# Performance work log

Hardware: AMD Instinct MI355X
Metric: run time of the kernel (lower is better)

The kernel has to match this reference:

```python
import jax, jax.numpy as jnp
import numpy as np

GROUPS = 32
EPS = 1e-5
NUM_HEADS = 8

def group_norm(x, scale, bias):
    # x: [N, C, T], GroupNorm(32) as in diffusion normalization()
    N, C, T = x.shape
    xg = x.reshape(N, GROUPS, -1)
    mean = xg.mean(-1, keepdims=True)
    var = xg.var(-1, keepdims=True)
    xg = (xg - mean) * jax.lax.rsqrt(var + EPS)
    return xg.reshape(N, C, T) * scale[None, :, None] + bias[None, :, None]


def setup_inputs() -> dict:
    key = jax.random.key(0)
    ks = jax.random.split(key, 10)
    B, D, C, T, TE = 2, 32, 256, 64, 1024
    s = 0.02
    inp = {}
    inp["x"] = jax.random.normal(ks[0], (B, D, C, T), jnp.float32)
    inp["temb"] = jax.random.normal(ks[1], (B, TE, T), jnp.float32)
    inp["frame_indices"] = jnp.sort(jax.random.randint(ks[2], (B, T), 0, 1000), axis=-1)
    inp["attn_mask"] = jnp.ones((B, T), jnp.float32)
    inp["norm_scale"] = jnp.ones((C,), jnp.float32)
    inp["norm_bias"] = jnp.zeros((C,), jnp.float32)
    inp["w_qkv"] = jax.random.normal(ks[3], (3 * C, C), jnp.float32) * s
    inp["b_qkv"] = jnp.zeros((3 * C,), jnp.float32)
    inp["w_aug1"] = jax.random.normal(ks[4], (C, 3), jnp.float32) * s
    inp["b_aug1"] = jnp.zeros((C,), jnp.float32)
    inp["w_aug2"] = jax.random.normal(ks[5], (C, TE), jnp.float32) * s
    inp["b_aug2"] = jnp.zeros((C,), jnp.float32)
    inp["w_aug3"] = jax.random.normal(ks[6], (C, C), jnp.float32) * s
    inp["b_aug3"] = jnp.zeros((C,), jnp.float32)
    inp["w_proj"] = jax.random.normal(ks[7], (C, C), jnp.float32) * s
    inp["b_proj"] = jnp.zeros((C,), jnp.float32)
    return inp


def reference(x, temb, frame_indices, attn_mask, norm_scale, norm_bias,
              w_qkv, b_qkv, w_aug1, b_aug1, w_aug2, b_aug2, w_aug3, b_aug3,
              w_proj, b_proj):
    B, D, C, T = x.shape
    H = NUM_HEADS
    cph = C // H  # channels per head
    # norm + 1x1 qkv conv over channels
    h = group_norm(x.reshape(B * D, C, T), norm_scale, norm_bias)
    qkv = jnp.einsum('nct,oc->not', h, w_qkv) + b_qkv[None, :, None]
    qkv = qkv.reshape(B, D, 3, cph, H, T)
    q, k, v = qkv[:, :, 0], qkv[:, :, 1], qkv[:, :, 2]
    scale = 1.0 / np.sqrt(np.sqrt(cph))
    w = jnp.einsum('bdcht,bdchs->bdhts', q * scale, k * scale)  # [B,D,H,T,T]
    # relative-position features: [B,3,T,T]
    rel = frame_indices[:, None, None, :] - frame_indices[:, None, :, None]
    rel3 = jnp.concatenate([
        jnp.clip(rel, 0, None).astype(jnp.float32),
        jnp.clip(-rel, 0, None).astype(jnp.float32),
        (rel == 0).astype(jnp.float32)], axis=1)
    rel3 = jnp.log1p(rel3)
    emb = jnp.einsum('bits,oi->bots', rel3, w_aug1) + b_aug1[None, :, None, None]  # [B,C,T,T]
    emb = emb + (jnp.einsum('bet,oe->bot', temb, w_aug2) + b_aug2[None, :, None])[:, :, :, None]
    wa = jnp.einsum('bits,oi->bots', jax.nn.relu(emb), w_aug3) + b_aug3[None, :, None, None]
    # tile heads into full channel dim (matches torch .repeat ordering) and add bias pre-softmax
    w = jnp.tile(w, (1, 1, cph, 1, 1)) + wa[:, None]  # [B,D,C,T,T]
    w = jnp.where(attn_mask[:, None, None, None, :] > 0, w, -jnp.inf)
    w = jax.nn.softmax(w.astype(jnp.float32), axis=-1).astype(x.dtype)
    hv = jnp.einsum('bdcts,bdcs->bdct', w, v.reshape(B, D, C, T))
    out = x + jnp.einsum('bdct,oc->bdot', hv, w_proj) + b_proj[None, None, :, None]
    return out
```

## Files before the change

### kernel.cpp

```cpp
#include <hip/hip_runtime.h>

#define B_ 2
#define D_ 32
#define C_ 256
#define T_ 64
#define TE_ 1024
#define H_ 8
#define N_ 64

typedef __attribute__((ext_vector_type(8))) short bf16x8;
typedef __attribute__((ext_vector_type(8))) unsigned short u16x8;
typedef __attribute__((ext_vector_type(4))) float f32x4;

__device__ inline ushort f2bf(float x){
  unsigned u = __float_as_uint(x);
  unsigned r = u + 0x7FFFu + ((u>>16)&1u);
  return (ushort)(r>>16);
}
__device__ inline float bf2f(ushort u){
  return __uint_as_float(((unsigned)u)<<16);
}

__global__ __launch_bounds__(256) void k_prep(
    const float* __restrict__ w_qkv, const float* __restrict__ wp,
    const float* __restrict__ w3,
    ushort* __restrict__ wqb, ushort* __restrict__ wpr, ushort* __restrict__ w3b,
    const float* __restrict__ x, const float* __restrict__ nsc,
    const float* __restrict__ nbi, ushort* __restrict__ ht,
    const float* __restrict__ temb, const float* __restrict__ w2,
    const float* __restrict__ b2, float* __restrict__ tp)
{
  __shared__ float smem[5120];
  int blk = blockIdx.x;
  int tid = threadIdx.x;
  if (blk < 320) {
    if (blk < 192) {
      int i = blk*256 + tid;
      float4 v = ((const float4*)w_qkv)[i];
      ushort4 o; o.x=f2bf(v.x); o.y=f2bf(v.y); o.z=f2bf(v.z); o.w=f2bf(v.w);
      ((ushort4*)wqb)[i] = o;
    } else if (blk < 256) {
      int i = (blk-192)*256 + tid;
      float4 v = ((const float4*)wp)[i];
      int o = i >> 6, c0 = (i & 63)*4;
      #pragma unroll
      for (int e=0;e<4;e++){
        int c = c0+e;
        float vv = (e==0)?v.x:(e==1)?v.y:(e==2)?v.z:v.w;
        wpr[o*256 + (c&7)*32 + (c>>3)] = f2bf(vv);
      }
    } else {
      int i = (blk-256)*256 + tid;
      float4 v = ((const float4*)w3)[i];
      ushort4 o; o.x=f2bf(v.x); o.y=f2bf(v.y); o.z=f2bf(v.z); o.w=f2bf(v.w);
      ((ushort4*)w3b)[i] = o;
    }
    return;
  }
  if (blk < 2368) {
    int b2k = blk - 320;
    int n = b2k >> 5, g = b2k & 31;
    const float* xp = x + ((size_t)n*C_ + g*8) * T_;
    float v0 = xp[tid], v1 = xp[tid+256];
    float s = v0+v1, ss = v0*v0 + v1*v1;
    #pragma unroll
    for (int off=32; off; off>>=1) { s += __shfl_down(s,off); ss += __shfl_down(ss,off); }
    float* red = smem;
    ushort* gbuf = (ushort*)(smem + 16);
    int wid = tid>>6, lane = tid&63;
    if (lane==0){ red[wid]=s; red[4+wid]=ss; }
    __syncthreads();
    if (tid==0){
      float a  = red[0]+red[1]+red[2]+red[3];
      float bb = red[4]+red[5]+red[6]+red[7];
      float mean = a*(1.f/512.f);
      float var  = bb*(1.f/512.f) - mean*mean;
      red[8]=mean; red[9]=rsqrtf(var + 1e-5f);
    }
    __syncthreads();
    float mean = red[8], inv = red[9];
    int t = tid & 63, w = tid >> 6;
    int c0 = g*8 + w, c1 = c0 + 4;
    gbuf[w*64 + t]     = f2bf((v0-mean)*inv*nsc[c0] + nbi[c0]);
    gbuf[(w+4)*64 + t] = f2bf((v1-mean)*inv*nsc[c1] + nbi[c1]);
    __syncthreads();
    if (tid < 64){
      u16x8 pk;
      #pragma unroll
      for (int i=0;i<8;i++) pk[i] = gbuf[i*64 + tid];
      *(u16x8*)&ht[((size_t)n*T_ + tid)*C_ + g*8] = pk;
    }
    return;
  }
  {
    int b3k = blk - 2368;
    int b = b3k >> 6, ob = b3k & 63;
    float* w2s = smem;
    float* red = smem + 4096;
    const float* w2p = w2 + (size_t)ob*4*1024;
    #pragma unroll
    for (int r = 0; r < 16; r++) w2s[r*256 + tid] = w2p[r*256 + tid];
    __syncthreads();
    int t = tid & 63, eq = tid >> 6;
    const float* tep = temb + ((size_t)b*1024 + eq*256)*64 + t;
    const float* wq  = w2s + eq*256;
    float acc[4] = {0.f,0.f,0.f,0.f};
    #pragma unroll 4
    for (int i = 0; i < 256; i += 4) {
      float tv0 = tep[(i+0)*64];
      float tv1 = tep[(i+1)*64];
      float tv2 = tep[(i+2)*64];
      float tv3 = tep[(i+3)*64];
      #pragma unroll
      for (int j = 0; j < 4; j++) {
        float4 w4 = *(const float4*)&wq[j*1024 + i];
        acc[j] = fmaf(w4.x, tv0, acc[j]);
        acc[j] = fmaf(w4.y, tv1, acc[j]);
        acc[j] = fmaf(w4.z, tv2, acc[j]);
        acc[j] = fmaf(w4.w, tv3, acc[j]);
      }
    }
    #pragma unroll
    for (int j=0;j<4;j++) red[(eq*4+j)*64 + t] = acc[j];
    __syncthreads();
    if (tid < 64) {
      #pragma unroll
      for (int j=0;j<4;j++){
        int o = ob*4 + j;
        float v = red[j*64+tid]+red[(4+j)*64+tid]+red[(8+j)*64+tid]+red[(12+j)*64+tid];
        tp[((size_t)b*256+o)*64 + tid] = v + b2[o];
      }
    }
  }
}

__global__ __launch_bounds__(256) void k_mm(
    const ushort* __restrict__ Wb, const ushort* __restrict__ Inb,
    const float* __restrict__ bias, ushort* __restrict__ Out)
{
  int blk = blockIdx.x;
  int n = blk / 12, ob = blk - n*12;
  int tid = threadIdx.x;
  int lane = tid & 63, w = tid >> 6;
  int o0 = ob*64 + w*16;
  int r = lane & 15, kg = lane >> 4;
  const ushort* wp = Wb + (size_t)(o0 + r)*256 + kg*8;
  const ushort* ip = Inb + ((size_t)n*64 + r)*256 + kg*8;
  f32x4 acc[4];
  #pragma unroll
  for (int j=0;j<4;j++) acc[j] = (f32x4){0.f,0.f,0.f,0.f};
  #pragma unroll
  for (int ks = 0; ks < 8; ks++) {
    bf16x8 a = *(const bf16x8*)(wp + ks*32);
    #pragma unroll
    for (int j = 0; j < 4; j++) {
      bf16x8 b = *(const bf16x8*)(ip + (size_t)j*16*256 + ks*32);
      acc[j] = __builtin_amdgcn_mfma_f32_16x16x32_bf16(a, b, acc[j], 0, 0, 0);
    }
  }
  #pragma unroll
  for (int j = 0; j < 4; j++) {
    #pragma unroll
    for (int rr = 0; rr < 4; rr++) {
      int o = o0 + kg*4 + rr;
      size_t idx = ((size_t)n*768 + o)*64 + j*16 + r;
      float v = acc[j][rr] + bias[o];
      if (o < 512) v *= 0.42044820762685725f;
      Out[idx] = f2bf(v);
    }
  }
}

__global__ __launch_bounds__(256) void k_sw(
    const ushort* __restrict__ qkv, ushort* __restrict__ es,
    const float* __restrict__ amask,
    const int* __restrict__ fi, const float* __restrict__ w1,
    const float* __restrict__ b1, const float* __restrict__ tp,
    const ushort* __restrict__ w3b, const float* __restrict__ b3,
    ushort* __restrict__ ew)
{
  __shared__ char smem[33536];
  int blk = blockIdx.x;
  int tid = threadIdx.x;
  if (blk < 512) {
    int n = blk >> 3, hh = blk & 7;
    float* qs = (float*)smem;
    float* ks = qs + 2048;
    const ushort* base = qkv + (size_t)n*(768*64);
    for (int i=tid; i<2048; i+=256){
      int cq = i>>6, tt = i&63;
      qs[i] = bf2f(base[(cq*8+hh)*64 + tt]);
      ks[i] = bf2f(base[(256 + cq*8+hh)*64 + tt]);
    }
    __syncthreads();
    int s  = tid & 63;
    int t4 = __builtin_amdgcn_readfirstlane(tid>>6);
    float msk = amask[(n >> 5)*64 + s];
    float acc[16];
    #pragma unroll
    for (int j=0;j<16;j++) acc[j]=0.f;
    for (int cq=0;cq<32;cq++){
      float kv = ks[cq*64+s];
      #pragma unroll
      for (int j=0;j<16;j++) acc[j] = fmaf(qs[cq*64 + t4*16 + j], kv, acc[j]);
    }
    ushort* op = es + (size_t)blk*4096;
    #pragma unroll
    for (int j=0;j<16;j++)
      op[(t4*16+j)*64 + s] = f2bf(msk > 0.f ? __expf(acc[j]) : 0.f);
    return;
  }
  {
    int blk2 = blk - 512;
    int oh = blk2 & 1; int bt = blk2 >> 1;
    int b = bt >> 6, t = bt & 63;
    float* l0 = (float*)smem;
    float* l1 = l0 + 64;
    float* l2 = l1 + 64;
    ushort* Ebuf = (ushort*)(smem + 768);
    if (tid < 64){
      int rel = fi[b*64+tid] - fi[b*64+t];
      float r0 = rel>0 ? (float)rel   : 0.f;
      float r1 = rel<0 ? (float)(-rel): 0.f;
      l0[tid] = log1pf(r0);
      l1[tid] = log1pf(r1);
      l2[tid] = (rel==0) ? 0.6931471805599453f : 0.f;
    }
    __syncthreads();
    int s = tid & 63;
    int iq = __builtin_amdgcn_readfirstlane(tid >> 6);
    float L0 = l0[s], L1 = l1[s], L2 = l2[s];
    #pragma unroll
    for (int c8 = 0; c8 < 8; c8++){
      int chunk = iq*8 + c8;
      int ibase = chunk*8;
      u16x8 pack;
      #pragma unroll
      for (int e = 0; e < 8; e++){
        int i = ibase + e;
        float bb = b1[i] + tp[((size_t)b*256 + i)*64 + t];
        float evv = fmaf(w1[i*3], L0, fmaf(w1[i*3+1], L1, fmaf(w1[i*3+2], L2, bb)));
        pack[e] = f2bf(fmaxf(evv, 0.f));
      }
      int csw = chunk ^ (s & 31);
      *(u16x8*)&Ebuf[s*256 + csw*8] = pack;
    }
    __syncthreads();
    int lane = tid & 63, w = tid >> 6;
    int r = lane & 15, kg = lane >> 4;
    int o0 = oh*128 + w*32;
    f32x4 acc[2][4];
    #pragma unroll
    for (int m=0;m<2;m++)
      #pragma unroll
      for (int j=0;j<4;j++) acc[m][j] = (f32x4){0.f,0.f,0.f,0.f};
    #pragma unroll
    for (int ks8 = 0; ks8 < 8; ks8++){
      bf16x8 a0 = *(const bf16x8*)(w3b + (size_t)(o0 +      r)*256 + kg*8 + ks8*32);
      bf16x8 a1 = *(const bf16x8*)(w3b + (size_t)(o0 + 16 + r)*256 + kg*8 + ks8*32);
      #pragma unroll
      for (int j=0;j<4;j++){
        int srow = j*16 + r;
        int chunk = (kg + ks8*4) ^ (srow & 31);
        bf16x8 bfr = *(const bf16x8*)&Ebuf[srow*256 + chunk*8];
        acc[0][j] = __builtin_amdgcn_mfma_f32_16x16x32_bf16(a0, bfr, acc[0][j], 0, 0, 0);
        acc[1][j] = __builtin_amdgcn_mfma_f32_16x16x32_bf16(a1, bfr, acc[1][j], 0, 0, 0);
      }
    }
    #pragma unroll
    for (int m=0;m<2;m++){
      #pragma unroll
      for (int j=0;j<4;j++){
        #pragma unroll
        for (int rr=0;rr<4;rr++){
          int o = o0 + m*16 + kg*4 + rr;
          int scol = j*16 + r;
          ew[((size_t)(b*256+o))*4096 + t*64 + scol] = f2bf(__expf(acc[m][j][rr] + b3[o]));
        }
      }
    }
  }
}

__global__ __launch_bounds__(256) void k_attn(
    const ushort* __restrict__ es, const ushort* __restrict__ ew,
    const ushort* __restrict__ qkv, ushort* __restrict__ hv1)
{
  int i = blockIdx.x;
  int xcd = i & 7, j0 = i >> 3;
  int g = xcd + ((j0 >> 6) << 3);
  int w64 = j0 & 63;
  int b = g >> 3, hh = g & 7;
  int dq = w64 >> 3, cs = w64 & 7;
  int tid = threadIdx.x;
  int t  = tid & 63;
  int dj = __builtin_amdgcn_readfirstlane(tid >> 6);
  int n  = b*D_ + dq*4 + dj;
  __shared__ float4 ewl[64][16];
  __shared__ float4 vl4[4][16];
  float4 esr[16];
  {
    const u16x8* sp = (const u16x8*)(es + ((size_t)(n*8 + hh))*4096 + (size_t)t*64);
    #pragma unroll
    for (int k8=0;k8<8;k8++){
      u16x8 e8 = sp[k8];
      float4 lo, hi;
      lo.x=bf2f(e8[0]); lo.y=bf2f(e8[1]); lo.z=bf2f(e8[2]); lo.w=bf2f(e8[3]);
      hi.x=bf2f(e8[4]); hi.y=bf2f(e8[5]); hi.z=bf2f(e8[6]); hi.w=bf2f(e8[7]);
      esr[2*k8] = lo; esr[2*k8+1] = hi;
    }
  }
  int vd = tid >> 4, vk = tid & 15;
  u16x8 rew[2]; ushort4 rv;
  {
    int c = cs*32 + hh;
    const u16x8* wap = (const u16x8*)(ew + ((size_t)(b*256 + c))*4096);
    rew[0] = wap[tid]; rew[1] = wap[tid+256];
    if (tid < 64)
      rv = *(const ushort4*)(qkv + ((size_t)(b*D_ + dq*4 + vd)*768 + 512 + c)*64 + 4*vk);
  }
  for (int ci=0; ci<4; ci++){
    __syncthreads();
    #pragma unroll
    for (int i2=0;i2<2;i2++){
      int ch = tid + 256*i2;
      int tr = ch >> 3, k8 = ch & 7;
      u16x8 e8 = rew[i2];
      float4 lo, hi;
      lo.x=bf2f(e8[0]); lo.y=bf2f(e8[1]); lo.z=bf2f(e8[2]); lo.w=bf2f(e8[3]);
      hi.x=bf2f(e8[4]); hi.y=bf2f(e8[5]); hi.z=bf2f(e8[6]); hi.w=bf2f(e8[7]);
      ewl[tr][(k8*2)   ^ (tr & 15)] = lo;
      ewl[tr][(k8*2+1) ^ (tr & 15)] = hi;
    }
    if (tid < 64){
      float4 vv; vv.x=bf2f(rv.x); vv.y=bf2f(rv.y); vv.z=bf2f(rv.z); vv.w=bf2f(rv.w);
      vl4[vd][vk] = vv;
    }
    __syncthreads();
    if (ci < 3){
      int c = (cs*4 + ci + 1)*8 + hh;
      const u16x8* wap = (const u16x8*)(ew + ((size_t)(b*256 + c))*4096);
      rew[0] = wap[tid]; rew[1] = wap[tid+256];
      if (tid < 64)
        rv = *(const ushort4*)(qkv + ((size_t)(b*D_ + dq*4 + vd)*768 + 512 + c)*64 + 4*vk);
    }
    float sum = 0.f;
    float ax=0.f, ay=0.f, az=0.f, aw=0.f;
    #pragma unroll
    for (int k=0;k<16;k++){
      float4 e4 = esr[k];
      float4 w4 = ewl[t][k ^ (t & 15)];
      float4 v4 = vl4[dj][k];
      float px = e4.x*w4.x, py = e4.y*w4.y, pz = e4.z*w4.z, pw = e4.w*w4.w;
      sum += px+py+pz+pw;
      ax = fmaf(px, v4.x, ax);
      ay = fmaf(py, v4.y, ay);
      az = fmaf(pz, v4.z, az);
      aw = fmaf(pw, v4.w, aw);
    }
    float acc = (ax+ay)+(az+aw);
    int cq = cs*4 + ci;
    hv1[(((size_t)n*8 + hh)*32 + cq)*64 + t] = f2bf(acc / sum);
  }
}

__global__ __launch_bounds__(256) void k_proj(
    const ushort* __restrict__ Wr, const ushort* __restrict__ hv1,
    const float* __restrict__ bias, const float* __restrict__ resid,
    float* __restrict__ Out)
{
  int blk = blockIdx.x;
  int n = blk >> 2, ob = blk & 3;
  int tid = threadIdx.x;
  int lane = tid & 63, w = tid >> 6;
  int o0 = ob*64 + w*16;
  int r = lane & 15, kg = lane >> 4;
  const ushort* wp = Wr + (size_t)(o0 + r)*256 + kg*8;
  f32x4 acc[4];
  #pragma unroll
  for (int j=0;j<4;j++) acc[j] = (f32x4){0.f,0.f,0.f,0.f};
  #pragma unroll
  for (int ks = 0; ks < 8; ks++) {
    bf16x8 a = *(const bf16x8*)(wp + ks*32);
    #pragma unroll
    for (int j = 0; j < 4; j++) {
      const ushort* bp = hv1 + (((size_t)n*8 + ks)*32 + kg*8)*64 + (j*16 + r);
      bf16x8 bfr;
      #pragma unroll
      for (int e=0;e<8;e++) bfr[e] = (short)bp[(size_t)e*64];
      acc[j] = __builtin_amdgcn_mfma_f32_16x16x32_bf16(a, bfr, acc[j], 0, 0, 0);
    }
  }
  #pragma unroll
  for (int j = 0; j < 4; j++) {
    #pragma unroll
    for (int rr = 0; rr < 4; rr++) {
      int o = o0 + kg*4 + rr;
      size_t idx = ((size_t)n*256 + o)*64 + j*16 + r;
      Out[idx] = acc[j][rr] + bias[o] + resid[idx];
    }
  }
}

extern "C" void kernel_launch(void* const* d_in, const int* in_sizes, int n_in,
                              void* d_out, int out_size, void* d_ws, size_t ws_size,
                              hipStream_t stream) {
  const float* x     = (const float*)d_in[0];
  const float* temb  = (const float*)d_in[1];
  const int*   fi    = (const int*)  d_in[2];
  const float* amask = (const float*)d_in[3];
  const float* nsc   = (const float*)d_in[4];
  const float* nbi   = (const float*)d_in[5];
  const float* w_qkv = (const float*)d_in[6];
  const float* b_qkv = (const float*)d_in[7];
  const float* w1    = (const float*)d_in[8];
  const float* b1    = (const float*)d_in[9];
  const float* w2    = (const float*)d_in[10];
  const float* b2    = (const float*)d_in[11];
  const float* w3    = (const float*)d_in[12];
  const float* b3    = (const float*)d_in[13];
  const float* wp    = (const float*)d_in[14];
  const float* bp    = (const float*)d_in[15];
  float* out = (float*)d_out;

  ushort* qkvb = (ushort*)d_ws;
  float*  tpb  = (float*)(qkvb + 3145728);
  ushort* esb  = (ushort*)(tpb + 32768);
  ushort* ewb  = esb + 2097152;
  ushort* htb  = ewb + 2097152;
  ushort* hvb  = htb + 1048576;
  ushort* wqb  = hvb + 1048576;
  ushort* wprb = wqb + 196608;
  ushort* w3b  = wprb + 65536;

  k_prep <<<2496, 256, 0, stream>>>(w_qkv, wp, w3, wqb, wprb, w3b,
                                    x, nsc, nbi, htb, temb, w2, b2, tpb);
  k_mm   <<<N_*12, 256, 0, stream>>>(wqb, htb, b_qkv, qkvb);
  k_sw   <<<768, 256, 0, stream>>>(qkvb, esb, amask, fi, w1, b1, tpb, w3b, b3, ewb);
  k_attn <<<B_*H_*8*8, 256, 0, stream>>>(esb, ewb, qkvb, hvb);
  k_proj <<<N_*4, 256, 0, stream>>>(wprb, hvb, bp, x, out);
}
```

Before: 64.49 us.

## Fuse QK score computation into attention kernel and merge QKV GEMM with bias kernel

The per-head QK^T exp scores are no longer computed in a separate pass and written to global memory. Each attention block now computes them with MFMA from the qkv buffer and stores them in XOR-swizzled shared memory. The QKV GEMM and the relative-position bias branch are merged into one launch, cutting one kernel launch and the es global round trip. The cost is that QK scores are recomputed by each of the 8 channel-slice blocks that share a head, and q/k are loaded with scalar strided gathers.

```diff
diff --git a/kernel.cpp b/kernel.cpp
--- a/kernel.cpp
+++ b/kernel.cpp
@@ -134,46 +134,9 @@
   }
 }
 
-__global__ __launch_bounds__(256) void k_mm(
+__global__ __launch_bounds__(256) void k_mw(
     const ushort* __restrict__ Wb, const ushort* __restrict__ Inb,
-    const float* __restrict__ bias, ushort* __restrict__ Out)
-{
-  int blk = blockIdx.x;
-  int n = blk / 12, ob = blk - n*12;
-  int tid = threadIdx.x;
-  int lane = tid & 63, w = tid >> 6;
-  int o0 = ob*64 + w*16;
-  int r = lane & 15, kg = lane >> 4;
-  const ushort* wp = Wb + (size_t)(o0 + r)*256 + kg*8;
-  const ushort* ip = Inb + ((size_t)n*64 + r)*256 + kg*8;
-  f32x4 acc[4];
-  #pragma unroll
-  for (int j=0;j<4;j++) acc[j] = (f32x4){0.f,0.f,0.f,0.f};
-  #pragma unroll
-  for (int ks = 0; ks < 8; ks++) {
-    bf16x8 a = *(const bf16x8*)(wp + ks*32);
-    #pragma unroll
-    for (int j = 0; j < 4; j++) {
-      bf16x8 b = *(const bf16x8*)(ip + (size_t)j*16*256 + ks*32);
-      acc[j] = __builtin_amdgcn_mfma_f32_16x16x32_bf16(a, b, acc[j], 0, 0, 0);
-    }
-  }
-  #pragma unroll
-  for (int j = 0; j < 4; j++) {
-    #pragma unroll
-    for (int rr = 0; rr < 4; rr++) {
-      int o = o0 + kg*4 + rr;
-      size_t idx = ((size_t)n*768 + o)*64 + j*16 + r;
-      float v = acc[j][rr] + bias[o];
-      if (o < 512) v *= 0.42044820762685725f;
-      Out[idx] = f2bf(v);
-    }
-  }
-}
-
-__global__ __launch_bounds__(256) void k_sw(
-    const ushort* __restrict__ qkv, ushort* __restrict__ es,
-    const float* __restrict__ amask,
+    const float* __restrict__ bias, ushort* __restrict__ Out,
     const int* __restrict__ fi, const float* __restrict__ w1,
     const float* __restrict__ b1, const float* __restrict__ tp,
     const ushort* __restrict__ w3b, const float* __restrict__ b3,
@@ -182,36 +145,40 @@
   __shared__ char smem[33536];
   int blk = blockIdx.x;
   int tid = threadIdx.x;
-  if (blk < 512) {
-    int n = blk >> 3, hh = blk & 7;
-    float* qs = (float*)smem;
-    float* ks = qs + 2048;
-    const ushort* base = qkv + (size_t)n*(768*64);
-    for (int i=tid; i<2048; i+=256){
-      int cq = i>>6, tt = i&63;
-      qs[i] = bf2f(base[(cq*8+hh)*64 + tt]);
-      ks[i] = bf2f(base[(256 + cq*8+hh)*64 + tt]);
-    }
-    __syncthreads();
-    int s  = tid & 63;
-    int t4 = __builtin_amdgcn_readfirstlane(tid>>6);
-    float msk = amask[(n >> 5)*64 + s];
-    float acc[16];
-    #pragma unroll
-    for (int j=0;j<16;j++) acc[j]=0.f;
-    for (int cq=0;cq<32;cq++){
-      float kv = ks[cq*64+s];
-      #pragma unroll
-      for (int j=0;j<16;j++) acc[j] = fmaf(qs[cq*64 + t4*16 + j], kv, acc[j]);
-    }
-    ushort* op = es + (size_t)blk*4096;
-    #pragma unroll
-    for (int j=0;j<16;j++)
-      op[(t4*16+j)*64 + s] = f2bf(msk > 0.f ? __expf(acc[j]) : 0.f);
+  if (blk < 768) {
+    int n = blk / 12, ob = blk - n*12;
+    int lane = tid & 63, w = tid >> 6;
+    int o0 = ob*64 + w*16;
+    int r = lane & 15, kg = lane >> 4;
+    const ushort* wp = Wb + (size_t)(o0 + r)*256 + kg*8;
+    const ushort* ip = Inb + ((size_t)n*64 + r)*256 + kg*8;
+    f32x4 acc[4];
+    #pragma unroll
+    for (int j=0;j<4;j++) acc[j] = (f32x4){0.f,0.f,0.f,0.f};
+    #pragma unroll
+    for (int ks = 0; ks < 8; ks++) {
+      bf16x8 a = *(const bf16x8*)(wp + ks*32);
+      #pragma unroll
+      for (int j = 0; j < 4; j++) {
+        bf16x8 b = *(const bf16x8*)(ip + (size_t)j*16*256 + ks*32);
+        acc[j] = __builtin_amdgcn_mfma_f32_16x16x32_bf16(a, b, acc[j], 0, 0, 0);
+      }
+    }
+    #pragma unroll
+    for (int j = 0; j < 4; j++) {
+      #pragma unroll
+      for (int rr = 0; rr < 4; rr++) {
+        int o = o0 + kg*4 + rr;
+        size_t idx = ((size_t)n*768 + o)*64 + j*16 + r;
+        float v = acc[j][rr] + bias[o];
+        if (o < 512) v *= 0.42044820762685725f;
+        Out[idx] = f2bf(v);
+      }
+    }
     return;
   }
   {
-    int blk2 = blk - 512;
+    int blk2 = blk - 768;
     int oh = blk2 & 1; int bt = blk2 >> 1;
     int b = bt >> 6, t = bt & 63;
     float* l0 = (float*)smem;
@@ -282,9 +249,9 @@
   }
 }
 
-__global__ __launch_bounds__(256) void k_attn(
-    const ushort* __restrict__ es, const ushort* __restrict__ ew,
-    const ushort* __restrict__ qkv, ushort* __restrict__ hv1)
+__global__ __launch_bounds__(256) void k_attn2(
+    const ushort* __restrict__ qkv, const ushort* __restrict__ ew,
+    const float* __restrict__ amask, ushort* __restrict__ hv1)
 {
   int i = blockIdx.x;
   int xcd = i & 7, j0 = i >> 3;
@@ -293,23 +260,64 @@
   int b = g >> 3, hh = g & 7;
   int dq = w64 >> 3, cs = w64 & 7;
   int tid = threadIdx.x;
-  int t  = tid & 63;
-  int dj = __builtin_amdgcn_readfirstlane(tid >> 6);
-  int n  = b*D_ + dq*4 + dj;
-  __shared__ float4 ewl[64][16];
-  __shared__ float4 vl4[4][16];
+  int lane = tid & 63;
+  int wid = __builtin_amdgcn_readfirstlane(tid >> 6);
+  int r = lane & 15, kg = lane >> 4;
+  int n = b*D_ + dq*4 + wid;
+
+  __shared__ __align__(16) char smem[33536];
+  ushort* esl = (ushort*)smem;
+  float4 (*ewl)[16] = (float4(*)[16])smem;
+  float4 (*vl4)[16] = (float4(*)[16])(smem + 16384);
+
+  {
+    const ushort* qb = qkv + (size_t)n*(768*64);
+    bf16x8 af[4], bfj[4];
+    #pragma unroll
+    for (int jt=0;jt<4;jt++){
+      #pragma unroll
+      for (int e=0;e<8;e++)
+        af[jt][e] = (short)qb[(((kg*8+e)*8 + hh)*64) + jt*16 + r];
+    }
+    #pragma unroll
+    for (int js=0;js<4;js++){
+      #pragma unroll
+      for (int e=0;e<8;e++)
+        bfj[js][e] = (short)qb[((256 + (kg*8+e)*8 + hh)*64) + js*16 + r];
+    }
+    float msk[4];
+    #pragma unroll
+    for (int js=0;js<4;js++) msk[js] = amask[b*64 + js*16 + r];
+    #pragma unroll
+    for (int jt=0;jt<4;jt++){
+      #pragma unroll
+      for (int js=0;js<4;js++){
+        f32x4 acc = (f32x4){0.f,0.f,0.f,0.f};
+        acc = __builtin_amdgcn_mfma_f32_16x16x32_bf16(af[jt], bfj[js], acc, 0, 0, 0);
+        int s = js*16 + r;
+        #pragma unroll
+        for (int rr=0;rr<4;rr++){
+          int t = jt*16 + kg*4 + rr;
+          float ev = msk[js] > 0.f ? __expf(acc[rr]) : 0.f;
+          esl[((wid*64 + t)<<6) + (((s>>3) ^ (t&7))<<3) + (s&7)] = f2bf(ev);
+        }
+      }
+    }
+  }
+  __syncthreads();
+  int t = lane;
   float4 esr[16];
-  {
-    const u16x8* sp = (const u16x8*)(es + ((size_t)(n*8 + hh))*4096 + (size_t)t*64);
-    #pragma unroll
-    for (int k8=0;k8<8;k8++){
-      u16x8 e8 = sp[k8];
-      float4 lo, hi;
-      lo.x=bf2f(e8[0]); lo.y=bf2f(e8[1]); lo.z=bf2f(e8[2]); lo.w=bf2f(e8[3]);
-      hi.x=bf2f(e8[4]); hi.y=bf2f(e8[5]); hi.z=bf2f(e8[6]); hi.w=bf2f(e8[7]);
-      esr[2*k8] = lo; esr[2*k8+1] = hi;
-    }
-  }
+  #pragma unroll
+  for (int k8=0;k8<8;k8++){
+    u16x8 e8 = *(const u16x8*)&esl[((wid*64 + t)<<6) + ((k8 ^ (t&7))<<3)];
+    float4 lo, hi;
+    lo.x=bf2f(e8[0]); lo.y=bf2f(e8[1]); lo.z=bf2f(e8[2]); lo.w=bf2f(e8[3]);
+    hi.x=bf2f(e8[4]); hi.y=bf2f(e8[5]); hi.z=bf2f(e8[6]); hi.w=bf2f(e8[7]);
+    esr[2*k8] = lo; esr[2*k8+1] = hi;
+  }
+  __syncthreads();
+
+  int dj = wid;
   int vd = tid >> 4, vk = tid & 15;
   u16x8 rew[2]; ushort4 rv;
   {
@@ -425,18 +433,17 @@
 
   ushort* qkvb = (ushort*)d_ws;
   float*  tpb  = (float*)(qkvb + 3145728);
-  ushort* esb  = (ushort*)(tpb + 32768);
-  ushort* ewb  = esb + 2097152;
+  ushort* ewb  = (ushort*)(tpb + 32768);
   ushort* htb  = ewb + 2097152;
   ushort* hvb  = htb + 1048576;
   ushort* wqb  = hvb + 1048576;
   ushort* wprb = wqb + 196608;
   ushort* w3b  = wprb + 65536;
 
-  k_prep <<<2496, 256, 0, stream>>>(w_qkv, wp, w3, wqb, wprb, w3b,
-                                    x, nsc, nbi, htb, temb, w2, b2, tpb);
-  k_mm   <<<N_*12, 256, 0, stream>>>(wqb, htb, b_qkv, qkvb);
-  k_sw   <<<768, 256, 0, stream>>>(qkvb, esb, amask, fi, w1, b1, tpb, w3b, b3, ewb);
-  k_attn <<<B_*H_*8*8, 256, 0, stream>>>(esb, ewb, qkvb, hvb);
-  k_proj <<<N_*4, 256, 0, stream>>>(wprb, hvb, bp, x, out);
-}
+  k_prep  <<<2496, 256, 0, stream>>>(w_qkv, wp, w3, wqb, wprb, w3b,
+                                     x, nsc, nbi, htb, temb, w2, b2, tpb);
+  k_mw    <<<1024, 256, 0, stream>>>(wqb, htb, b_qkv, qkvb,
+                                     fi, w1, b1, tpb, w3b, b3, ewb);
+  k_attn2 <<<1024, 256, 0, stream>>>(qkvb, ewb, amask, hvb);
+  k_proj  <<<N_*4, 256, 0, stream>>>(wprb, hvb, bp, x, out);
+}
```

Result: faster. 62.20 us, median of 2 (-3.5%).
